# Kernel optimization log

Measured on AMD Instinct MI355X. Metric: run time of the kernel, lower is better.

## Reference

```python
import jax, jax.numpy as jnp
import numpy as np

NINP, NHID, K = 300, 64, 2   # input dim, hidden dim, pyramid levels (from Net.__init__)
GH = NHID // K               # per-pyramid-level width contributed to each gate (32)
S, B = 512, 256              # seq_len, batch


def setup_inputs() -> dict:
    key = jax.random.key(0)
    k = jax.random.split(key, 5)
    s = 0.05
    return {
        "x": jax.random.normal(k[0], (S, B, NINP), jnp.float32),
        "h0": jnp.zeros((B, NHID), jnp.float32),
        "c0": jnp.zeros((B, NHID), jnp.float32),
        "W_pt0": jax.random.normal(k[1], (NINP, 4 * GH), jnp.float32) * s,
        "b_pt0": jnp.zeros((4 * GH,), jnp.float32),
        "W_pt1": jax.random.normal(k[2], (NINP // 2, 4 * GH), jnp.float32) * s,
        "b_pt1": jnp.zeros((4 * GH,), jnp.float32),
        "W_glt": jax.random.normal(k[3], (1, NHID, 4 * NHID), jnp.float32) * s,  # g=1 grouped linear
        "W_dec": jax.random.normal(k[4], (NHID, 3), jnp.float32) * s,
        "b_dec": jnp.zeros((3,), jnp.float32),
    }


def _pyramidal_i2h(x, W_pt0, b_pt0, W_pt1, b_pt1):
    # Pyramidal transform: level 0 = full-res input, level 1 = features avg-pooled by 2.
    # Each level produces 4*GH gate features; levels are concatenated per gate -> NHID.
    x1 = x.reshape(x.shape[0], x.shape[1], NINP // 2, 2).mean(-1)  # (S,B,150)
    g0 = (x @ W_pt0 + b_pt0).reshape(x.shape[0], x.shape[1], 4, GH)
    g1 = (x1 @ W_pt1 + b_pt1).reshape(x.shape[0], x.shape[1], 4, GH)
    return jnp.concatenate([g0, g1], axis=-1)  # (S,B,4,NHID) gates order: f,g,i,o


def reference(x, h0, c0, W_pt0, b_pt0, W_pt1, b_pt1, W_glt, W_dec, b_dec):
    # Precompute input-to-hidden gate contributions for all timesteps (same math as per-step).
    i2h = _pyramidal_i2h(x, W_pt0, b_pt0, W_pt1, b_pt1)  # (S,B,4,NHID)
    bsz = h0.shape[0]

    def step(carry, i2h_t):
        h, c = carry
        # grouped linear (g=1): (B,1,NHID) x (1,NHID,4*NHID) -> (B,4,NHID)
        h2h = jnp.einsum('bgi,gio->bgo', h.reshape(bsz, 1, NHID), W_glt).reshape(bsz, 4, NHID)
        gates = i2h_t + h2h
        f, g, i, o = gates[:, 0], gates[:, 1], gates[:, 2], gates[:, 3]
        c1 = jax.nn.sigmoid(f) * c + jax.nn.sigmoid(i) * jnp.tanh(g)
        h1 = jax.nn.sigmoid(o) * jnp.tanh(c1)
        return (h1, c1), h1

    (hT, cT), hs = jax.lax.scan(step, (h0, c0), i2h)  # hs: (S,B,NHID)
    decoded = hs @ W_dec + b_dec                       # (S,B,3)
    return decoded, hT, cT
```

## Files before the change

kernel.cpp:

```cpp
#include <hip/hip_runtime.h>
#include <hip/hip_bf16.h>

#define SLEN 512
#define BATCH 256
#define NIN 300
#define KP 320
#define NG 256
#define NH 64
#define BM 128
#define BN 128
#define BK 64
#define LDP 72
#define TC 128
#define NCH (SLEN / TC)

typedef float f32x4 __attribute__((ext_vector_type(4)));
typedef _Float16 f16x8 __attribute__((ext_vector_type(8)));
typedef _Float16 f16x4 __attribute__((ext_vector_type(4)));

template <int J>
__device__ __forceinline__ float quad_bcast(float v) {
  return __builtin_bit_cast(float,
      __builtin_amdgcn_mov_dpp(__builtin_bit_cast(int, v),
                               J * 0x55, 0xf, 0xf, true));
}

__global__ void prep_w(const float* __restrict__ Wpt0, const float* __restrict__ bpt0,
                       const float* __restrict__ Wpt1, const float* __restrict__ bpt1,
                       const float* __restrict__ Wglt,
                       _Float16* __restrict__ Wc16, float* __restrict__ bcat,
                       _Float16* __restrict__ Wg16) {
  int idx = blockIdx.x * 256 + threadIdx.x;
  if (idx < NG * KP) {
    int n = idx / KP, k = idx - n * KP;
    int g = n >> 6, h = n & 63;
    float w = 0.f;
    if (k < NIN) {
      if (h < 32) w = Wpt0[k * 128 + g * 32 + h];
      else        w = 0.5f * Wpt1[(k >> 1) * 128 + g * 32 + (h - 32)];
    }
    Wc16[idx] = (_Float16)w;
  }
  if (idx < NG * NH) {
    int c = idx >> 6, k = idx & 63;
    Wg16[idx] = (_Float16)Wglt[k * NG + c];
  }
  if (idx < NG) {
    int g = idx >> 6, h = idx & 63;
    bcat[idx] = (h < 32) ? bpt0[g * 32 + h] : bpt1[g * 32 + h - 32];
  }
}


__device__ __forceinline__ void gemm_body(
    char* LB, int m0, int n0, int tid,
    const float* __restrict__ x, const _Float16* __restrict__ Wc16,
    const float* __restrict__ bcat, _Float16* __restrict__ C) {
  _Float16 (*As)[LDP] = reinterpret_cast<_Float16(*)[LDP]>(LB);
  _Float16 (*Bs)[LDP] = reinterpret_cast<_Float16(*)[LDP]>(LB + BM * LDP * 2);
  const int lane = tid & 63;
  const int w = tid >> 6;
  const int wr = w >> 1, wc = w & 1;

  f32x4 acc[4][4];
#pragma unroll
  for (int m = 0; m < 4; ++m)
#pragma unroll
    for (int n = 0; n < 4; ++n) acc[m][n] = (f32x4){0.f, 0.f, 0.f, 0.f};

  const int arow_l = tid >> 4;
  const int acol   = (tid & 15) * 4;
  const int brow_l = tid >> 3;
  const int bcol   = (tid & 7) * 8;

  for (int k0 = 0; k0 < KP; k0 += BK) {
#pragma unroll
    for (int p = 0; p < 8; ++p) {
      int row = p * 16 + arow_l;
      int gk = k0 + acol;
      f32x4 v = (f32x4){0.f, 0.f, 0.f, 0.f};
      if (gk + 3 < NIN)
        v = *reinterpret_cast<const f32x4*>(&x[(size_t)(m0 + row) * NIN + gk]);
      f16x4 sv;
      sv[0] = (_Float16)v[0]; sv[1] = (_Float16)v[1];
      sv[2] = (_Float16)v[2]; sv[3] = (_Float16)v[3];
      *reinterpret_cast<f16x4*>(&As[row][acol]) = sv;
    }
#pragma unroll
    for (int p = 0; p < 4; ++p) {
      int n = p * 32 + brow_l;
      f16x8 v = *reinterpret_cast<const f16x8*>(&Wc16[(size_t)(n0 + n) * KP + k0 + bcol]);
      *reinterpret_cast<f16x8*>(&Bs[n][bcol]) = v;
    }
    __syncthreads();
#pragma unroll
    for (int ks = 0; ks < 2; ++ks) {
      const int kk = ks * 32 + (lane >> 4) * 8;
      f16x8 a[4], b[4];
#pragma unroll
      for (int m = 0; m < 4; ++m)
        a[m] = *reinterpret_cast<const f16x8*>(&As[wr * 64 + m * 16 + (lane & 15)][kk]);
#pragma unroll
      for (int n = 0; n < 4; ++n)
        b[n] = *reinterpret_cast<const f16x8*>(&Bs[wc * 64 + n * 16 + (lane & 15)][kk]);
#pragma unroll
      for (int m = 0; m < 4; ++m)
#pragma unroll
        for (int n = 0; n < 4; ++n)
          acc[m][n] = __builtin_amdgcn_mfma_f32_16x16x32_f16(a[m], b[n], acc[m][n], 0, 0, 0);
    }
    __syncthreads();
  }
  const int fc = lane & 15;
  const int fr = (lane >> 4) * 4;
#pragma unroll
  for (int n = 0; n < 4; ++n) {
    int col = n0 + wc * 64 + n * 16 + fc;
    float bias = bcat[col];
#pragma unroll
    for (int m = 0; m < 4; ++m) {
#pragma unroll
      for (int r = 0; r < 4; ++r) {
        int row = m0 + wr * 64 + m * 16 + fr + r;
        C[(size_t)row * NG + col] = (_Float16)(acc[m][n][r] + bias);
      }
    }
  }
}

__device__ __forceinline__ void decode_body(
    char* LB, int blk, int tid,
    const _Float16* __restrict__ hs, const float* __restrict__ Wdec,
    const float* __restrict__ bdec, float* __restrict__ out) {
  float* wl = reinterpret_cast<float*>(LB);
  float* bl = reinterpret_cast<float*>(LB + 768);
  float* ob = reinterpret_cast<float*>(LB + 784);
  if (tid < NH * 3) wl[tid] = Wdec[tid];
  if (tid < 3) bl[tid] = bdec[tid];
  __syncthreads();
  const size_t idx = (size_t)blk * 256 + tid;
  const _Float16* hp = hs + idx * NH;
  float d0 = 0.f, d1 = 0.f, d2 = 0.f;
#pragma unroll
  for (int k = 0; k < NH; k += 8) {
    f16x8 h8 = *reinterpret_cast<const f16x8*>(&hp[k]);
#pragma unroll
    for (int j = 0; j < 8; ++j) {
      float hv = (float)h8[j];
      d0 += hv * wl[(k + j) * 3 + 0];
      d1 += hv * wl[(k + j) * 3 + 1];
      d2 += hv * wl[(k + j) * 3 + 2];
    }
  }
  ob[tid * 3 + 0] = d0 + bl[0];
  ob[tid * 3 + 1] = d1 + bl[1];
  ob[tid * 3 + 2] = d2 + bl[2];
  __syncthreads();
  if (tid < 192) {
    f32x4* o4 = reinterpret_cast<f32x4*>(out + (size_t)blk * 768);
    o4[tid] = reinterpret_cast<const f32x4*>(ob)[tid];
  }
}

#define PAIR(v, j) __builtin_shufflevector(v, v, 2*(j), 2*(j)+1)
#define DOT(hb, i, W) { f16x8 hv = (hb)[i]; \
      acc0 = __builtin_amdgcn_fdot2(PAIR(hv,0), PAIR(W,0), acc0, false); \
      acc1 = __builtin_amdgcn_fdot2(PAIR(hv,1), PAIR(W,1), acc1, false); \
      acc0 = __builtin_amdgcn_fdot2(PAIR(hv,2), PAIR(W,2), acc0, false); \
      acc1 = __builtin_amdgcn_fdot2(PAIR(hv,3), PAIR(W,3), acc1, false); }

#define STEP(CUR, SP) { \
    float cur_ = (float)__builtin_bit_cast(_Float16, (unsigned short)(CUR)); \
    const f16x8* hb = reinterpret_cast<const f16x8*>(hbuf + ((SP) & 1) * NH); \
    float acc0 = 0.f, acc1 = 0.f; \
    DOT(hb, 0, w0) DOT(hb, 1, w1) DOT(hb, 2, w2) DOT(hb, 3, w3) \
    DOT(hb, 4, w4) DOT(hb, 5, w5) DOT(hb, 6, w6) DOT(hb, 7, w7) \
    float pre = cur_ + (acc0 + acc1); \
    float xx = fminf(fmaxf(pre, -30.f), 30.f); \
    float e = __expf(-mm * xx); \
    float y = 1.f / (1.f + e); \
    float act = (qid == 1) ? (2.f * y - 1.f) : y; \
    float f_ = quad_bcast<0>(act); \
    float g_ = quad_bcast<1>(act); \
    float i_ = quad_bcast<2>(act); \
    float o_ = quad_bcast<3>(act); \
    float c1 = f_ * creg + i_ * g_;    \
    creg = c1; \
    float ct = fminf(fmaxf(c1, -15.f), 15.f); \
    float e2 = __expf(-2.f * ct); \
    float th = (1.f - e2) / (1.f + e2); \
    float h1 = o_ * th; \
    hreg = h1; \
    if (qid == 0) { \
      hbuf[(((SP) + 1) & 1) * NH + unit] = (_Float16)h1; \
      *hp = (_Float16)h1;   \
    } \
    hp += st >> 2;  \
    asm volatile("s_waitcnt lgkmcnt(0)" ::: "memory"); \
    __builtin_amdgcn_s_barrier(); }


__global__ __launch_bounds__(256, 2) void gemm_i2h(
    const float* __restrict__ x, const _Float16* __restrict__ Wc16,
    const float* __restrict__ bcat, _Float16* __restrict__ C) {
  __shared__ __align__(16) char LB[36864];
  gemm_body(LB, blockIdx.y * BM, blockIdx.x * BN, threadIdx.x, x, Wc16, bcat, C);
}

__global__ __launch_bounds__(256) void decode(
    const _Float16* __restrict__ hs, const float* __restrict__ Wdec,
    const float* __restrict__ bdec, float* __restrict__ out) {
  __shared__ __align__(16) char LB[4096];
  decode_body(LB, blockIdx.x, threadIdx.x, hs, Wdec, bdec, out);
}

__global__ __launch_bounds__(256, 2)
void fused_step(
    const _Float16* __restrict__ i2h_cur, _Float16* __restrict__ i2h_next,
    const float* __restrict__ x_next,
    const _Float16* __restrict__ Wc16, const float* __restrict__ bcat,
    const _Float16* __restrict__ Wg16,
    const float* __restrict__ h_in, const float* __restrict__ c_in,
    float* __restrict__ h_state, float* __restrict__ c_state,
    _Float16* __restrict__ hs_cur, const _Float16* __restrict__ hs_prev,
    const float* __restrict__ Wdec, const float* __restrict__ bdec,
    float* __restrict__ out_prev,
    float* __restrict__ hT_out, float* __restrict__ cT_out,
    int is_last, int has_gemm) {
  __shared__ __align__(16) char LB[36864];
  const int bid = blockIdx.x;
  const int tid = threadIdx.x;

  if (bid < BATCH) {
    const int b = bid;
    const int ww = tid >> 6;
    const int l = tid & 63;
    const int qid = l & 3;
    const int unit = ww * 16 + (l >> 2);
    const int col = qid * 64 + unit;

    f16x8* Wst = reinterpret_cast<f16x8*>(LB);
    _Float16* hbuf = reinterpret_cast<_Float16*>(LB);

    for (int e = tid; e < 8 * NG; e += 256) {
      int kk = e >> 8, c = e & 255;
      Wst[e] = *reinterpret_cast<const f16x8*>(Wg16 + (size_t)c * NH + kk * 8);
    }
    __syncthreads();

    f16x8 w0 = Wst[0 * NG + col], w1 = Wst[1 * NG + col];
    f16x8 w2 = Wst[2 * NG + col], w3 = Wst[3 * NG + col];
    f16x8 w4 = Wst[4 * NG + col], w5 = Wst[5 * NG + col];
    f16x8 w6 = Wst[6 * NG + col], w7 = Wst[7 * NG + col];

    float creg = c_in[b * NH + unit];
    float hreg = 0.f;
    float h0v = (tid < NH) ? h_in[b * NH + tid] : 0.f;
    __syncthreads();

    if (tid < NH) hbuf[tid] = (_Float16)h0v;
    __syncthreads();

    __builtin_amdgcn_s_setprio(1);

    const size_t st = (size_t)NG * BATCH;
    const unsigned short* ip =
        reinterpret_cast<const unsigned short*>(i2h_cur) + (size_t)b * NG + col;
    _Float16* hp = hs_cur + (size_t)b * NH + unit;
    const float mm = (qid == 1) ? 2.f : 1.f;

    int s = 0;
    {
      unsigned short c0v = ip[0],      c1v = ip[st],     c2v = ip[2 * st], c3v = ip[3 * st];
      unsigned short n0v = ip[4 * st], n1v = ip[5 * st], n2v = ip[6 * st], n3v = ip[7 * st];
      const unsigned short* ipf = ip + 8 * st;
      while (s + 4 <= TC) {
        unsigned short f0v = 0, f1v = 0, f2v = 0, f3v = 0;
        if (s + 8  < TC) f0v = ipf[0];
        if (s + 9  < TC) f1v = ipf[st];
        if (s + 10 < TC) f2v = ipf[2 * st];
        if (s + 11 < TC) f3v = ipf[3 * st];
        ipf += 4 * st;
        STEP(c0v, s)
        STEP(c1v, s + 1)
        STEP(c2v, s + 2)
        STEP(c3v, s + 3)
        c0v = n0v; c1v = n1v; c2v = n2v; c3v = n3v;
        n0v = f0v; n1v = f1v; n2v = f2v; n3v = f3v;
        s += 4;
      }
    }
    __builtin_amdgcn_s_setprio(0);

    if (qid == 0) {
      h_state[b * NH + unit] = hreg;
      c_state[b * NH + unit] = creg;
      if (is_last) {
        hT_out[b * NH + unit] = hreg;
        cT_out[b * NH + unit] = creg;
      }
    }
  } else if (has_gemm && bid < BATCH + 2 * (TC * BATCH / BM)) {
    const int gid = bid - BATCH;
    const int n0 = (gid & 1) * BN;
    const int m0 = (gid >> 1) * BM;
    gemm_body(LB, m0, n0, tid, x_next, Wc16, bcat, i2h_next);
  } else {
    const int did = bid - BATCH - (has_gemm ? 2 * (TC * BATCH / BM) : 0);
    decode_body(LB, did, tid, hs_prev, Wdec, bdec, out_prev);
  }
}

extern "C" void kernel_launch(void* const* d_in, const int* in_sizes, int n_in,
                              void* d_out, int out_size, void* d_ws, size_t ws_size,
                              hipStream_t stream) {
  const float* x    = (const float*)d_in[0];
  const float* h0   = (const float*)d_in[1];
  const float* c0   = (const float*)d_in[2];
  const float* Wpt0 = (const float*)d_in[3];
  const float* bpt0 = (const float*)d_in[4];
  const float* Wpt1 = (const float*)d_in[5];
  const float* bpt1 = (const float*)d_in[6];
  const float* Wglt = (const float*)d_in[7];
  const float* Wdec = (const float*)d_in[8];
  const float* bdec = (const float*)d_in[9];
  float* out = (float*)d_out;

  char* ws = (char*)d_ws;
  _Float16*  Wc16    = (_Float16*)(ws);
  float*     bcat    = (float*)(ws + 163840);
  _Float16*  Wg16    = (_Float16*)(ws + 164864);
  float*     h_state = (float*)(ws + 197632);
  float*     c_state = (float*)(ws + 263168);
  const size_t base = 328704;

  const size_t chunk_i2h = (size_t)TC * BATCH * NG;
  _Float16* i2h0 = (_Float16*)(ws + base);
  _Float16* i2h1 = i2h0 + chunk_i2h;
  _Float16* hs   = (_Float16*)(ws + base + 4 * chunk_i2h);

  prep_w<<<dim3((NG * KP + 255) / 256), dim3(256), 0, stream>>>(
      Wpt0, bpt0, Wpt1, bpt1, Wglt, Wc16, bcat, Wg16);

  gemm_i2h<<<dim3(2, TC * BATCH / BM), dim3(256), 0, stream>>>(
      x, Wc16, bcat, i2h0);

  for (int k = 0; k < NCH; ++k) {
    _Float16* cur = (k & 1) ? i2h1 : i2h0;
    _Float16* nxt = (k & 1) ? i2h0 : i2h1;
    const int has_gemm = (k + 1 < NCH) ? 1 : 0;
    const int has_dec  = (k > 0) ? 1 : 0;
    const int nblk = BATCH + (has_gemm ? 2 * (TC * BATCH / BM) : 0)
                           + (has_dec ? (TC * BATCH / 256) : 0);
    const int kp = (k > 0) ? (k - 1) : 0;
    fused_step<<<dim3(nblk), dim3(256), 0, stream>>>(
        cur, nxt, x + (size_t)(k + 1) * TC * BATCH * NIN,
        Wc16, bcat, Wg16,
        (k == 0) ? h0 : h_state, (k == 0) ? c0 : c_state,
        h_state, c_state,
        hs + (size_t)k * TC * BATCH * NH,
        hs + (size_t)kp * TC * BATCH * NH,
        Wdec, bdec,
        out + (size_t)kp * TC * BATCH * 3,
        out + (size_t)SLEN * BATCH * 3,
        out + (size_t)SLEN * BATCH * 3 + BATCH * NH,
        (k == NCH - 1) ? 1 : 0, has_gemm);
  }

  decode<<<dim3(TC * BATCH / 256), dim3(256), 0, stream>>>(
      hs + (size_t)(NCH - 1) * TC * BATCH * NH, Wdec, bdec,
      out + (size_t)(NCH - 1) * TC * BATCH * 3);
}
```

Measured before the change: 247.3 us.

## Remap recurrent step so two lanes cover four gates, halving active waves

The recurrent part of fused_step now maps each hidden unit to a lane pair instead of a quad. Each lane computes two gate columns with interleaved fdot2 chains (f/i or g/o), exchanges them through a single DPP pair swap, and only waves 0-1 do work. Waves 2-3 just match the per-step barriers. The aim is to cut the per-step barrier and wave synchronisation cost and the DPP broadcast count. In exchange each active lane holds twice the weight registers and does twice the dot-product work, which lengthens the serial chain per step.

```diff
diff --git a/kernel.cpp b/kernel.cpp
--- a/kernel.cpp
+++ b/kernel.cpp
@@ -18,11 +18,9 @@
 typedef _Float16 f16x8 __attribute__((ext_vector_type(8)));
 typedef _Float16 f16x4 __attribute__((ext_vector_type(4)));
 
-template <int J>
-__device__ __forceinline__ float quad_bcast(float v) {
+__device__ __forceinline__ float pair_swap(float v) {
   return __builtin_bit_cast(float,
-      __builtin_amdgcn_mov_dpp(__builtin_bit_cast(int, v),
-                               J * 0x55, 0xf, 0xf, true));
+      __builtin_amdgcn_mov_dpp(__builtin_bit_cast(int, v), 0xB1, 0xf, 0xf, true));
 }
 
 __global__ void prep_w(const float* __restrict__ Wpt0, const float* __restrict__ bpt0,
@@ -163,27 +161,34 @@
 }
 
 #define PAIR(v, j) __builtin_shufflevector(v, v, 2*(j), 2*(j)+1)
-#define DOT(hb, i, W) { f16x8 hv = (hb)[i]; \
-      acc0 = __builtin_amdgcn_fdot2(PAIR(hv,0), PAIR(W,0), acc0, false); \
-      acc1 = __builtin_amdgcn_fdot2(PAIR(hv,1), PAIR(W,1), acc1, false); \
-      acc0 = __builtin_amdgcn_fdot2(PAIR(hv,2), PAIR(W,2), acc0, false); \
-      acc1 = __builtin_amdgcn_fdot2(PAIR(hv,3), PAIR(W,3), acc1, false); }
-
-#define STEP(CUR, SP) { \
-    float cur_ = (float)__builtin_bit_cast(_Float16, (unsigned short)(CUR)); \
+#define DOTW(KK) { f16x8 hv = hb[KK]; \
+    aA0 = __builtin_amdgcn_fdot2(PAIR(hv,0), PAIR(wa##KK,0), aA0, false); \
+    aB0 = __builtin_amdgcn_fdot2(PAIR(hv,0), PAIR(wb##KK,0), aB0, false); \
+    aA1 = __builtin_amdgcn_fdot2(PAIR(hv,1), PAIR(wa##KK,1), aA1, false); \
+    aB1 = __builtin_amdgcn_fdot2(PAIR(hv,1), PAIR(wb##KK,1), aB1, false); \
+    aA0 = __builtin_amdgcn_fdot2(PAIR(hv,2), PAIR(wa##KK,2), aA0, false); \
+    aB0 = __builtin_amdgcn_fdot2(PAIR(hv,2), PAIR(wb##KK,2), aB0, false); \
+    aA1 = __builtin_amdgcn_fdot2(PAIR(hv,3), PAIR(wa##KK,3), aA1, false); \
+    aB1 = __builtin_amdgcn_fdot2(PAIR(hv,3), PAIR(wb##KK,3), aB1, false); }
+
+#define STEP2W(CA, CB, SP) { \
+    float preA = (float)__builtin_bit_cast(_Float16, (unsigned short)(CA)); \
+    float preB = (float)__builtin_bit_cast(_Float16, (unsigned short)(CB)); \
     const f16x8* hb = reinterpret_cast<const f16x8*>(hbuf + ((SP) & 1) * NH); \
-    float acc0 = 0.f, acc1 = 0.f; \
-    DOT(hb, 0, w0) DOT(hb, 1, w1) DOT(hb, 2, w2) DOT(hb, 3, w3) \
-    DOT(hb, 4, w4) DOT(hb, 5, w5) DOT(hb, 6, w6) DOT(hb, 7, w7) \
-    float pre = cur_ + (acc0 + acc1); \
-    float xx = fminf(fmaxf(pre, -30.f), 30.f); \
-    float e = __expf(-mm * xx); \
-    float y = 1.f / (1.f + e); \
-    float act = (qid == 1) ? (2.f * y - 1.f) : y; \
-    float f_ = quad_bcast<0>(act); \
-    float g_ = quad_bcast<1>(act); \
-    float i_ = quad_bcast<2>(act); \
-    float o_ = quad_bcast<3>(act); \
+    float aA0 = 0.f, aA1 = 0.f, aB0 = 0.f, aB1 = 0.f; \
+    DOTW(0) DOTW(1) DOTW(2) DOTW(3) DOTW(4) DOTW(5) DOTW(6) DOTW(7) \
+    preA += aA0 + aA1; preB += aB0 + aB1; \
+    float xA = fminf(fmaxf(preA, -30.f), 30.f); \
+    float sA = 1.f / (1.f + __expf(-xA));             \
+    float xB = fminf(fmaxf(preB, -clB), clB); \
+    float yB = 1.f / (1.f + __expf(-mmB * xB)); \
+    float actB = gp ? yB : (2.f * yB - 1.f);          \
+    float sAo = pair_swap(sA); \
+    float aBo = pair_swap(actB); \
+    float f_ = gp ? sAo : sA; \
+    float g_ = gp ? aBo : actB; \
+    float i_ = gp ? sA : sAo; \
+    float o_ = gp ? actB : aBo; \
     float c1 = f_ * creg + i_ * g_;    \
     creg = c1; \
     float ct = fminf(fmaxf(c1, -15.f), 15.f); \
@@ -191,11 +196,11 @@
     float th = (1.f - e2) / (1.f + e2); \
     float h1 = o_ * th; \
     hreg = h1; \
-    if (qid == 0) { \
-      hbuf[(((SP) + 1) & 1) * NH + unit] = (_Float16)h1; \
+    if (gp == 0) { \
+      hbuf[(((SP) + 1) & 1) * NH + u] = (_Float16)h1; \
       *hp = (_Float16)h1;   \
     } \
-    hp += st >> 2;  \
+    hp += (size_t)BATCH * NH; \
     asm volatile("s_waitcnt lgkmcnt(0)" ::: "memory"); \
     __builtin_amdgcn_s_barrier(); }
 
@@ -233,14 +238,17 @@
 
   if (bid < BATCH) {
     const int b = bid;
-    const int ww = tid >> 6;
+    const int wv = tid >> 6;
     const int l = tid & 63;
-    const int qid = l & 3;
-    const int unit = ww * 16 + (l >> 2);
-    const int col = qid * 64 + unit;
+    const int gp = l & 1;
+    const int u = (wv & 1) * 32 + (l >> 1);
+    const int colA = gp * 128 + u;
+    const int colB = colA + 64;
 
     f16x8* Wst = reinterpret_cast<f16x8*>(LB);
-    _Float16* hbuf = reinterpret_cast<_Float16*>(LB);
+    unsigned hoff = 0;
+    asm volatile("" : "+s"(hoff));
+    _Float16* hbuf = reinterpret_cast<_Float16*>(LB + hoff);
 
     for (int e = tid; e < 8 * NG; e += 256) {
       int kk = e >> 8, c = e & 255;
@@ -248,12 +256,12 @@
     }
     __syncthreads();
 
-    f16x8 w0 = Wst[0 * NG + col], w1 = Wst[1 * NG + col];
-    f16x8 w2 = Wst[2 * NG + col], w3 = Wst[3 * NG + col];
-    f16x8 w4 = Wst[4 * NG + col], w5 = Wst[5 * NG + col];
-    f16x8 w6 = Wst[6 * NG + col], w7 = Wst[7 * NG + col];
-
-    float creg = c_in[b * NH + unit];
+#define LWA(KK) f16x8 wa##KK = Wst[(KK) * NG + colA];
+#define LWB(KK) f16x8 wb##KK = Wst[(KK) * NG + colB];
+    LWA(0) LWA(1) LWA(2) LWA(3) LWA(4) LWA(5) LWA(6) LWA(7)
+    LWB(0) LWB(1) LWB(2) LWB(3) LWB(4) LWB(5) LWB(6) LWB(7)
+
+    float creg = c_in[b * NH + u];
     float hreg = 0.f;
     float h0v = (tid < NH) ? h_in[b * NH + tid] : 0.f;
     __syncthreads();
@@ -261,43 +269,63 @@
     if (tid < NH) hbuf[tid] = (_Float16)h0v;
     __syncthreads();
 
-    __builtin_amdgcn_s_setprio(1);
-
-    const size_t st = (size_t)NG * BATCH;
-    const unsigned short* ip =
-        reinterpret_cast<const unsigned short*>(i2h_cur) + (size_t)b * NG + col;
-    _Float16* hp = hs_cur + (size_t)b * NH + unit;
-    const float mm = (qid == 1) ? 2.f : 1.f;
-
-    int s = 0;
-    {
-      unsigned short c0v = ip[0],      c1v = ip[st],     c2v = ip[2 * st], c3v = ip[3 * st];
-      unsigned short n0v = ip[4 * st], n1v = ip[5 * st], n2v = ip[6 * st], n3v = ip[7 * st];
-      const unsigned short* ipf = ip + 8 * st;
-      while (s + 4 <= TC) {
-        unsigned short f0v = 0, f1v = 0, f2v = 0, f3v = 0;
-        if (s + 8  < TC) f0v = ipf[0];
-        if (s + 9  < TC) f1v = ipf[st];
-        if (s + 10 < TC) f2v = ipf[2 * st];
-        if (s + 11 < TC) f3v = ipf[3 * st];
-        ipf += 4 * st;
-        STEP(c0v, s)
-        STEP(c1v, s + 1)
-        STEP(c2v, s + 2)
-        STEP(c3v, s + 3)
-        c0v = n0v; c1v = n1v; c2v = n2v; c3v = n3v;
-        n0v = f0v; n1v = f1v; n2v = f2v; n3v = f3v;
-        s += 4;
+    if (wv < 2) {
+      __builtin_amdgcn_s_setprio(1);
+      const size_t st = (size_t)NG * BATCH;
+      const unsigned short* ipA =
+          reinterpret_cast<const unsigned short*>(i2h_cur) + (size_t)b * NG + colA;
+      const unsigned short* ipB = ipA + 64;
+      _Float16* hp = hs_cur + (size_t)b * NH + u;
+      const float mmB = gp ? 1.f : 2.f;
+      const float clB = gp ? 30.f : 15.f;
+
+      int s = 0;
+      {
+        unsigned short c0a = ipA[0],      c0b = ipB[0];
+        unsigned short c1a = ipA[st],     c1b = ipB[st];
+        unsigned short c2a = ipA[2 * st], c2b = ipB[2 * st];
+        unsigned short c3a = ipA[3 * st], c3b = ipB[3 * st];
+        unsigned short n0a = ipA[4 * st], n0b = ipB[4 * st];
+        unsigned short n1a = ipA[5 * st], n1b = ipB[5 * st];
+        unsigned short n2a = ipA[6 * st], n2b = ipB[6 * st];
+        unsigned short n3a = ipA[7 * st], n3b = ipB[7 * st];
+        const unsigned short* ifA = ipA + 8 * st;
+        const unsigned short* ifB = ipB + 8 * st;
+        while (s + 4 <= TC) {
+          unsigned short f0a = 0, f0b = 0, f1a = 0, f1b = 0;
+          unsigned short f2a = 0, f2b = 0, f3a = 0, f3b = 0;
+          if (s + 8  < TC) { f0a = ifA[0];      f0b = ifB[0]; }
+          if (s + 9  < TC) { f1a = ifA[st];     f1b = ifB[st]; }
+          if (s + 10 < TC) { f2a = ifA[2 * st]; f2b = ifB[2 * st]; }
+          if (s + 11 < TC) { f3a = ifA[3 * st]; f3b = ifB[3 * st]; }
+          ifA += 4 * st; ifB += 4 * st;
+          STEP2W(c0a, c0b, s)
+          STEP2W(c1a, c1b, s + 1)
+          STEP2W(c2a, c2b, s + 2)
+          STEP2W(c3a, c3b, s + 3)
+          c0a = n0a; c0b = n0b; c1a = n1a; c1b = n1b;
+          c2a = n2a; c2b = n2b; c3a = n3a; c3b = n3b;
+          n0a = f0a; n0b = f0b; n1a = f1a; n1b = f1b;
+          n2a = f2a; n2b = f2b; n3a = f3a; n3b = f3b;
+          s += 4;
+        }
       }
-    }
-    __builtin_amdgcn_s_setprio(0);
-
-    if (qid == 0) {
-      h_state[b * NH + unit] = hreg;
-      c_state[b * NH + unit] = creg;
-      if (is_last) {
-        hT_out[b * NH + unit] = hreg;
-        cT_out[b * NH + unit] = creg;
+      __builtin_amdgcn_s_setprio(0);
+
+      if (gp == 0) {
+        h_state[b * NH + u] = hreg;
+        c_state[b * NH + u] = creg;
+        if (is_last) {
+          hT_out[b * NH + u] = hreg;
+          cT_out[b * NH + u] = creg;
+        }
+      }
+    } else {
+      for (int s2 = 0; s2 + 4 <= TC; s2 += 4) {
+        __builtin_amdgcn_s_barrier();
+        __builtin_amdgcn_s_barrier();
+        __builtin_amdgcn_s_barrier();
+        __builtin_amdgcn_s_barrier();
       }
     }
   } else if (has_gemm && bid < BATCH + 2 * (TC * BATCH / BM)) {
```

Result: slower. 308.2 us (+24.6%).
